# Kernel optimization log

Measured on AMD Instinct MI355X. Metric: run time of the kernel, lower is better.

Reference implementation:

```python
import jax, jax.numpy as jnp
import numpy as np

B, T, D = 2, 2048, 2048
H, HKV, RD = 16, 4, 64
DH = D // H          # 128
REP = H // HKV       # 4
NEG = -1e30


def _apply_rope(x, cos, sin, rd):
    # x: (B, h, T, Dh); cos/sin: (T, rd//2) broadcast over (B, h)
    xr, xp = x[..., :rd], x[..., rd:]
    x1, x2 = xr[..., ::2], xr[..., 1::2]
    rot = jnp.stack([x1 * cos - x2 * sin, x1 * sin + x2 * cos], axis=-1)
    rot = rot.reshape(x1.shape[:-1] + (rd,))
    return jnp.concatenate([rot, xp], axis=-1)


def setup_inputs() -> dict:
    key = jax.random.key(0)
    ks = jax.random.split(key, 6)
    x = jax.random.normal(ks[0], (B, T, D), dtype=jnp.float32)
    # rotary tables for the first RD dims (RD//2 frequency pairs)
    inv_freq = 1.0 / (10000.0 ** (np.arange(RD // 2, dtype=np.float32) / (RD // 2)))
    ang = np.arange(T, dtype=np.float32)[:, None] * inv_freq[None, :]  # (T, RD//2)
    cos = jnp.asarray(np.cos(ang), dtype=jnp.float32)
    sin = jnp.asarray(np.sin(ang), dtype=jnp.float32)
    s = 0.02
    Wq = jax.random.normal(ks[1], (H * DH, D), dtype=jnp.float32) * s
    Wk = jax.random.normal(ks[2], (HKV * DH, D), dtype=jnp.float32) * s
    Wv = jax.random.normal(ks[3], (HKV * DH, D), dtype=jnp.float32) * s
    Wo = jax.random.normal(ks[4], (D, D), dtype=jnp.float32) * s
    temp = jnp.full((H,), 1.0 / np.sqrt(DH), dtype=jnp.float32)
    return {"x": x, "cos": cos, "sin": sin, "Wq": Wq, "Wk": Wk, "Wv": Wv, "Wo": Wo, "temp": temp}


def reference(x, cos, sin, Wq, Wk, Wv, Wo, temp):
    Bt, Tt, _ = x.shape
    q = (x @ Wq.T).reshape(Bt, Tt, H, DH).transpose(0, 2, 1, 3)    # (B,H,T,Dh)
    k = (x @ Wk.T).reshape(Bt, Tt, HKV, DH).transpose(0, 2, 1, 3)  # (B,Hkv,T,Dh)
    v = (x @ Wv.T).reshape(Bt, Tt, HKV, DH).transpose(0, 2, 1, 3)
    k = jnp.repeat(k, REP, axis=1)  # GQA repeat_interleave -> (B,H,T,Dh)
    v = jnp.repeat(v, REP, axis=1)
    q = _apply_rope(q, cos, sin, RD)
    k = _apply_rope(k, cos, sin, RD)
    q = q * temp[None, :, None, None]
    # SDPA causal, with default 1/sqrt(Dh) scale on top of learned temp
    scores = jnp.einsum("bhqd,bhkd->bhqk", q, k) / np.sqrt(DH)
    causal = jnp.tril(jnp.ones((Tt, Tt), dtype=bool))
    scores = jnp.where(causal[None, None], scores, NEG)
    attn = jax.nn.softmax(scores, axis=-1)
    out = jnp.einsum("bhqk,bhkd->bhqd", attn, v)  # (B,H,T,Dh)
    out = out.transpose(0, 2, 1, 3).reshape(Bt, Tt, H * DH)
    return out @ Wo.T
```

## Files before the change

### kernel.cpp

```cpp
#include <hip/hip_runtime.h>
#include <hip/hip_bf16.h>
#include <math.h>

#define B_   2
#define T_   2048
#define D_   2048
#define H_   16
#define HKV_ 4
#define DH_  128
#define RD_  64
#define KD_  (HKV_ * DH_)
#define SQKV 3072
#define VOFF 2560

typedef __attribute__((ext_vector_type(8))) short  short8;
typedef __attribute__((ext_vector_type(4))) short  short4v;
typedef __attribute__((ext_vector_type(4))) float  floatx4;

__device__ __forceinline__ void async16(const __hip_bfloat16* g, __hip_bfloat16* l) {
  __builtin_amdgcn_global_load_lds(
      (const __attribute__((address_space(1))) void*)g,
      (__attribute__((address_space(3))) void*)l, 16, 0, 0);
}

__device__ __forceinline__ short bf16b(float x) {
  union { __hip_bfloat16 h; short s; } u;
  u.h = __float2bfloat16(x);
  return u.s;
}

struct ConvArgs {
  const float* src[5];
  __hip_bfloat16* dst[5];
  int n[5];
};

__global__ __launch_bounds__(256) void conv_bf16(ConvArgs a) {
  const int arr = blockIdx.y;
  const int i = (blockIdx.x * 256 + threadIdx.x) * 8;
  if (i >= a.n[arr]) return;
  const float4 f1 = *(const float4*)(a.src[arr] + i);
  const float4 f2 = *(const float4*)(a.src[arr] + i + 4);
  union { short8 v; __hip_bfloat16 h[8]; } o;
  o.h[0] = __float2bfloat16(f1.x); o.h[1] = __float2bfloat16(f1.y);
  o.h[2] = __float2bfloat16(f1.z); o.h[3] = __float2bfloat16(f1.w);
  o.h[4] = __float2bfloat16(f2.x); o.h[5] = __float2bfloat16(f2.y);
  o.h[6] = __float2bfloat16(f2.z); o.h[7] = __float2bfloat16(f2.w);
  *(short8*)(a.dst[arr] + i) = o.v;
}

template <int MODE>
__global__ __launch_bounds__(512, 2) void gemm_8ph(const __hip_bfloat16* __restrict__ A,
                                                   const __hip_bfloat16* __restrict__ Bw,
                                                   void* __restrict__ Cout,
                                                   __hip_bfloat16* __restrict__ vtout,
                                                   int M, int N, int K, int nwg_x) {
  __shared__ __hip_bfloat16 As[3][16 * 512];
  __shared__ __hip_bfloat16 Bs[3][16 * 512];

  const int tid  = threadIdx.x;
  const int lane = tid & 63;
  const int w    = tid >> 6;
  const int wm   = w >> 2, wn = w & 3;
  const int quad = lane >> 4, m16 = lane & 15;

  const int nwg = gridDim.x;
  const int q8  = nwg >> 3, r8 = nwg & 7;
  const int xcd = blockIdx.x & 7, o8 = blockIdx.x >> 3;
  const int swz = (xcd < r8 ? xcd * (q8 + 1) : r8 * (q8 + 1) + (xcd - r8) * q8) + o8;
  const int bx = swz % nwg_x, by = swz / nwg_x;
  const int bm = by * 256, bn = bx * 256;

  const int rl = m16;
  const int kc = quad;
  const __hip_bfloat16* gA0 = A  + (size_t)(bm + (w * 2 + 0) * 16 + rl) * K + kc * 8;
  const __hip_bfloat16* gA1 = A  + (size_t)(bm + (w * 2 + 1) * 16 + rl) * K + kc * 8;
  const __hip_bfloat16* gB0 = Bw + (size_t)(bn + (w * 2 + 0) * 16 + rl) * K + kc * 8;
  const __hip_bfloat16* gB1 = Bw + (size_t)(bn + (w * 2 + 1) * 16 + rl) * K + kc * 8;

  const int nt = K >> 5;

  async16(gA0,      &As[0][(w * 2 + 0) * 512]);
  async16(gA1,      &As[0][(w * 2 + 1) * 512]);
  async16(gB0,      &Bs[0][(w * 2 + 0) * 512]);
  async16(gB1,      &Bs[0][(w * 2 + 1) * 512]);
  async16(gA0 + 32, &As[1][(w * 2 + 0) * 512]);
  async16(gA1 + 32, &As[1][(w * 2 + 1) * 512]);
  async16(gB0 + 32, &Bs[1][(w * 2 + 0) * 512]);
  async16(gB1 + 32, &Bs[1][(w * 2 + 1) * 512]);

  floatx4 acc[8][4] = {};
  const int fragoff = (quad * 16 + m16) * 8;

  int cur = 0, stg = 2;
  for (int t = 0; t < nt; ++t) {
    if (t < nt - 1) asm volatile("s_waitcnt vmcnt(4)" ::: "memory");
    else            asm volatile("s_waitcnt vmcnt(0)" ::: "memory");
    __builtin_amdgcn_s_barrier();
    __builtin_amdgcn_sched_barrier(0);

    const __hip_bfloat16* abase = &As[cur][0];
    const __hip_bfloat16* bbase = &Bs[cur][0];
    const bool doStage = (t + 2 < nt);
    const size_t ko = (size_t)(t + 2) * 32;

    short8 a0[4], b[4];
#pragma unroll
    for (int i = 0; i < 4; ++i) {
      a0[i] = *(const short8*)(abase + (wm * 8 + i) * 512 + fragoff);
      b[i]  = *(const short8*)(bbase + (wn * 4 + i) * 512 + fragoff);
    }
    if (doStage) {
      async16(gA0 + ko, &As[stg][(w * 2 + 0) * 512]);
      async16(gA1 + ko, &As[stg][(w * 2 + 1) * 512]);
    }
    __builtin_amdgcn_s_barrier();
    __builtin_amdgcn_sched_barrier(0);
    __builtin_amdgcn_s_setprio(1);
#pragma unroll
    for (int i = 0; i < 4; ++i)
#pragma unroll
      for (int j = 0; j < 4; ++j)
        acc[i][j] = __builtin_amdgcn_mfma_f32_16x16x32_bf16(a0[i], b[j], acc[i][j], 0, 0, 0);
    __builtin_amdgcn_s_setprio(0);
    __builtin_amdgcn_s_barrier();
    __builtin_amdgcn_sched_barrier(0);

    short8 a1[4];
#pragma unroll
    for (int i = 0; i < 4; ++i)
      a1[i] = *(const short8*)(abase + (wm * 8 + 4 + i) * 512 + fragoff);
    if (doStage) {
      async16(gB0 + ko, &Bs[stg][(w * 2 + 0) * 512]);
      async16(gB1 + ko, &Bs[stg][(w * 2 + 1) * 512]);
    }
    __builtin_amdgcn_s_barrier();
    __builtin_amdgcn_sched_barrier(0);
    __builtin_amdgcn_s_setprio(1);
#pragma unroll
    for (int i = 0; i < 4; ++i)
#pragma unroll
      for (int j = 0; j < 4; ++j)
        acc[4 + i][j] = __builtin_amdgcn_mfma_f32_16x16x32_bf16(a1[i], b[j], acc[4 + i][j], 0, 0, 0);
    __builtin_amdgcn_s_setprio(0);

    cur = (cur == 2) ? 0 : cur + 1;
    stg = (stg == 2) ? 0 : stg + 1;
  }

  if (MODE == 2 && bn >= VOFF) {
#pragma unroll
    for (int mt = 0; mt < 8; ++mt)
#pragma unroll
      for (int j = 0; j < 4; ++j) {
        const int dh = bn + wn * 64 + j * 16 + m16 - VOFF;
        const int row0 = bm + wm * 128 + mt * 16 + quad * 4;
        const int bb = row0 >> 11, t0 = row0 & (T_ - 1);
        short4v pk;
#pragma unroll
        for (int reg = 0; reg < 4; ++reg) pk[reg] = bf16b(acc[mt][j][reg]);
        *(short4v*)&vtout[((size_t)(bb * HKV_ + (dh >> 7)) * DH_ + (dh & 127)) * T_ + t0] = pk;
      }
    return;
  }

#pragma unroll
  for (int mt = 0; mt < 8; ++mt)
#pragma unroll
    for (int j = 0; j < 4; ++j)
#pragma unroll
      for (int reg = 0; reg < 4; ++reg) {
        const int row = bm + wm * 128 + mt * 16 + quad * 4 + reg;
        const int col = bn + wn * 64 + j * 16 + m16;
        if (MODE == 0)
          ((float*)Cout)[(size_t)row * N + col] = acc[mt][j][reg];
        else
          ((__hip_bfloat16*)Cout)[(size_t)row * N + col] = __float2bfloat16(acc[mt][j][reg]);
      }
}

__global__ __launch_bounds__(512, 2) void gemm_k1(const __hip_bfloat16* __restrict__ A,
                                                  const __hip_bfloat16* __restrict__ Bw,
                                                  float* __restrict__ Cout,
                                                  int M, int N, int K, int nwg_x) {
  __shared__ __hip_bfloat16 As[3][8 * 512];
  __shared__ __hip_bfloat16 Bs[3][16 * 512];

  const int tid  = threadIdx.x;
  const int lane = tid & 63;
  const int w    = tid >> 6;
  const int wm   = w >> 2, wn = w & 3;
  const int quad = lane >> 4, m16 = lane & 15;

  const int nwg = gridDim.x;
  const int q8  = nwg >> 3, r8 = nwg & 7;
  const int xcd = blockIdx.x & 7, o8 = blockIdx.x >> 3;
  const int swz = (xcd < r8 ? xcd * (q8 + 1) : r8 * (q8 + 1) + (xcd - r8) * q8) + o8;
  const int bx = swz % nwg_x, by = swz / nwg_x;
  const int bm = by * 128, bn = bx * 256;

  const __hip_bfloat16* gA  = A  + (size_t)(bm + w * 16 + m16) * K + quad * 8;
  const __hip_bfloat16* gB0 = Bw + (size_t)(bn + (w * 2 + 0) * 16 + m16) * K + quad * 8;
  const __hip_bfloat16* gB1 = Bw + (size_t)(bn + (w * 2 + 1) * 16 + m16) * K + quad * 8;

  const int nt = K >> 5;

  async16(gA,       &As[0][w * 512]);
  async16(gB0,      &Bs[0][(w * 2 + 0) * 512]);
  async16(gB1,      &Bs[0][(w * 2 + 1) * 512]);
  async16(gA + 32,  &As[1][w * 512]);
  async16(gB0 + 32, &Bs[1][(w * 2 + 0) * 512]);
  async16(gB1 + 32, &Bs[1][(w * 2 + 1) * 512]);

  floatx4 acc[4][4] = {};
  const int fragoff = (quad * 16 + m16) * 8;

  int cur = 0, stg = 2;
  for (int t = 0; t < nt; ++t) {
    if (t < nt - 1) asm volatile("s_waitcnt vmcnt(3)" ::: "memory");
    else            asm volatile("s_waitcnt vmcnt(0)" ::: "memory");
    __builtin_amdgcn_s_barrier();
    __builtin_amdgcn_sched_barrier(0);

    const __hip_bfloat16* abase = &As[cur][0];
    const __hip_bfloat16* bbase = &Bs[cur][0];

    short8 a[4], b[4];
#pragma unroll
    for (int i = 0; i < 4; ++i) {
      a[i] = *(const short8*)(abase + (wm * 4 + i) * 512 + fragoff);
      b[i] = *(const short8*)(bbase + (wn * 4 + i) * 512 + fragoff);
    }
    if (t + 2 < nt) {
      const size_t ko = (size_t)(t + 2) * 32;
      async16(gA + ko,  &As[stg][w * 512]);
      async16(gB0 + ko, &Bs[stg][(w * 2 + 0) * 512]);
      async16(gB1 + ko, &Bs[stg][(w * 2 + 1) * 512]);
    }
    __builtin_amdgcn_s_setprio(1);
#pragma unroll
    for (int i = 0; i < 4; ++i)
#pragma unroll
      for (int j = 0; j < 4; ++j)
        acc[i][j] = __builtin_amdgcn_mfma_f32_16x16x32_bf16(a[i], b[j], acc[i][j], 0, 0, 0);
    __builtin_amdgcn_s_setprio(0);

    cur = (cur == 2) ? 0 : cur + 1;
    stg = (stg == 2) ? 0 : stg + 1;
  }

#pragma unroll
  for (int mi = 0; mi < 4; ++mi)
#pragma unroll
    for (int nj = 0; nj < 4; ++nj)
#pragma unroll
      for (int reg = 0; reg < 4; ++reg) {
        const int row = bm + wm * 64 + mi * 16 + quad * 4 + reg;
        const int col = bn + wn * 64 + nj * 16 + m16;
        Cout[(size_t)row * N + col] = acc[mi][nj][reg];
      }
}

__global__ __launch_bounds__(256) void rope_qk(__hip_bfloat16* __restrict__ qkv,
                                               const float* __restrict__ cosT,
                                               const float* __restrict__ sinT,
                                               const float* __restrict__ temp,
                                               float inv_sqrt_dh) {
  const int unit = blockIdx.x * 4 + (threadIdx.x >> 6);
  const int lane = threadIdx.x & 63;
  const int M = B_ * T_;
  int bt, off;
  float scale;
  if (unit < M * H_) {
    const int h = unit % H_;
    bt = unit / H_;
    off = h * DH_;
    scale = temp[h] * inv_sqrt_dh;
  } else {
    const int u2 = unit - M * H_;
    const int h = u2 % HKV_;
    bt = u2 / HKV_;
    off = D_ + h * DH_;
    scale = 1.0f;
  }
  const int t = bt & (T_ - 1);
  __hip_bfloat16* p = qkv + (size_t)bt * SQKV + off;
  if (lane < 32) {
    const float x1 = __bfloat162float(p[2 * lane]);
    const float x2 = __bfloat162float(p[2 * lane + 1]);
    const float c = cosT[t * (RD_ / 2) + lane];
    const float s = sinT[t * (RD_ / 2) + lane];
    p[2 * lane]     = __float2bfloat16((x1 * c - x2 * s) * scale);
    p[2 * lane + 1] = __float2bfloat16((x1 * s + x2 * c) * scale);
  } else {
    const int d0 = RD_ + (lane - 32) * 2;
    p[d0]     = __float2bfloat16(__bfloat162float(p[d0]) * scale);
    p[d0 + 1] = __float2bfloat16(__bfloat162float(p[d0 + 1]) * scale);
  }
}

__global__ __launch_bounds__(512, 2) void flash_attn_t2(
    const __hip_bfloat16* __restrict__ qkv,
    const __hip_bfloat16* __restrict__ vt,
    __hip_bfloat16* __restrict__ ao) {
  __shared__ __hip_bfloat16 KV[2][16384];

  const int tid = threadIdx.x, lane = tid & 63, w = tid >> 6;
  const int quad = lane >> 4, m16 = lane & 15;

  const int bid = blockIdx.x;
  const int g = bid & 7;
  const int b = g >> 2, kvh = g & 3;
  const int u = bid >> 3;
  const int qt = 63 - u;
  const int hw = w & 3;
  const int khalf = w >> 2;
  const int h = kvh * 4 + hw;
  const int qRow0 = qt * 32;
  const int ktEnd = (qt >> 1) + 1;

  const size_t bT = (size_t)b * T_;

  short8 qa[2][4];
#pragma unroll
  for (int qi = 0; qi < 2; qi++) {
    const __hip_bfloat16* qp = qkv + (bT + qRow0 + qi * 16 + m16) * SQKV + h * DH_;
#pragma unroll
    for (int ks = 0; ks < 4; ks++) qa[qi][ks] = *(const short8*)(qp + ks * 32 + quad * 8);
  }

  const short one = (short)0x3F80;
  const short4v ones4 = {one, one, one, one};

  const __hip_bfloat16* kptr[2];
  const __hip_bfloat16* vptr[2];
#pragma unroll
  for (int e = 0; e < 2; e++) {
    const int I = w * 2 + e;
    const int panelK = I >> 2, kcK = (I & 3) * 4 + quad;
    kptr[e] = qkv + D_ + (bT + panelK * 16 + m16) * SQKV + kvh * DH_ + kcK * 8;
    const int panelV = I >> 1, tc = (I & 1) * 4 + quad;
    vptr[e] = vt + ((size_t)(b * HKV_ + kvh) * DH_ + panelV * 16 + m16) * T_ + tc * 8;
  }

#pragma unroll
  for (int e = 0; e < 2; e++) {
    const int I = w * 2 + e;
    async16(kptr[e], &KV[0][I * 512]);
    async16(vptr[e], &KV[0][8192 + I * 512]);
    kptr[e] += (size_t)64 * SQKV;
    vptr[e] += 64;
  }

  floatx4 ot[8][2] = {};
  floatx4 lt[2] = {};

  for (int kt = 0; kt < ktEnd; kt++) {
    const int cur = kt & 1;
    __syncthreads();
    if (kt + 1 < ktEnd) {
      const int nxt = cur ^ 1;
#pragma unroll
      for (int e = 0; e < 2; e++) {
        const int I = w * 2 + e;
        async16(kptr[e], &KV[nxt][I * 512]);
        async16(vptr[e], &KV[nxt][8192 + I * 512]);
        kptr[e] += (size_t)64 * SQKV;
        vptr[e] += 64;
      }
    }

    const bool last = (kt == ktEnd - 1);
    if (last && khalf == 1 && ((qt & 1) == 0)) continue;

    floatx4 st[2][2] = {};
#pragma unroll
    for (int ki = 0; ki < 2; ki++) {
      const int kg = khalf * 2 + ki;
#pragma unroll
      for (int ks = 0; ks < 4; ks++) {
        const int unit = kg * 256 + (ks * 4 + quad) * 16 + m16;
        const short8 kf = *(const short8*)&KV[cur][unit * 8];
#pragma unroll
        for (int qi = 0; qi < 2; qi++)
          st[ki][qi] = __builtin_amdgcn_mfma_f32_16x16x32_bf16(kf, qa[qi][ks],
                                                               st[ki][qi], 0, 0, 0);
      }
    }

    if (last && khalf == (qt & 1)) {
#pragma unroll
      for (int ki = 0; ki < 2; ki++)
#pragma unroll
        for (int qi = 0; qi < 2; qi++) {
          const int rowg = qRow0 + qi * 16 + m16;
#pragma unroll
          for (int reg = 0; reg < 4; reg++) {
            const int keyg = kt * 64 + khalf * 32 + ki * 16 + quad * 4 + reg;
            if (keyg > rowg) st[ki][qi][reg] = -1e30f;
          }
        }
    }

    short4v pf[2][2];
#pragma unroll
    for (int ki = 0; ki < 2; ki++)
#pragma unroll
      for (int qi = 0; qi < 2; qi++) {
        short4v t;
#pragma unroll
        for (int reg = 0; reg < 4; reg++) t[reg] = bf16b(__expf(st[ki][qi][reg]));
        pf[ki][qi] = t;
      }

#pragma unroll
    for (int mi = 0; mi < 8; mi++)
#pragma unroll
      for (int ki = 0; ki < 2; ki++) {
        const int kg = khalf * 2 + ki;
        const int unit = mi * 128 + (kg * 2 + (quad >> 1)) * 16 + m16;
        const short4v vf = *(const short4v*)&KV[cur][8192 + unit * 8 + (quad & 1) * 4];
#pragma unroll
        for (int qi = 0; qi < 2; qi++)
          ot[mi][qi] = __builtin_amdgcn_mfma_f32_16x16x16bf16_1k(vf, pf[ki][qi],
                                                                 ot[mi][qi], 0, 0, 0);
      }
#pragma unroll
    for (int ki = 0; ki < 2; ki++)
#pragma unroll
      for (int qi = 0; qi < 2; qi++)
        lt[qi] = __builtin_amdgcn_mfma_f32_16x16x16bf16_1k(ones4, pf[ki][qi],
                                                           lt[qi], 0, 0, 0);
  }

  floatx4* scr = (floatx4*)&KV[0][0];
  __syncthreads();
  if (khalf == 1) {
#pragma unroll
    for (int mi = 0; mi < 6; mi++)
#pragma unroll
      for (int qi = 0; qi < 2; qi++)
        scr[((hw * 6 + mi) * 2 + qi) * 64 + lane] = ot[mi][qi];
  }
  __syncthreads();
  if (khalf == 0) {
#pragma unroll
    for (int mi = 0; mi < 6; mi++)
#pragma unroll
      for (int qi = 0; qi < 2; qi++)
        ot[mi][qi] += scr[((hw * 6 + mi) * 2 + qi) * 64 + lane];
  }
  __syncthreads();
  if (khalf == 1) {
#pragma unroll
    for (int j = 0; j < 2; j++)
#pragma unroll
      for (int qi = 0; qi < 2; qi++)
        scr[((hw * 2 + j) * 2 + qi) * 64 + lane] = ot[6 + j][qi];
#pragma unroll
    for (int qi = 0; qi < 2; qi++)
      scr[1024 + (hw * 2 + qi) * 64 + lane] = lt[qi];
  }
  __syncthreads();
  if (khalf == 0) {
#pragma unroll
    for (int j = 0; j < 2; j++)
#pragma unroll
      for (int qi = 0; qi < 2; qi++)
        ot[6 + j][qi] += scr[((hw * 2 + j) * 2 + qi) * 64 + lane];
#pragma unroll
    for (int qi = 0; qi < 2; qi++)
      lt[qi] += scr[1024 + (hw * 2 + qi) * 64 + lane];

#pragma unroll
    for (int qi = 0; qi < 2; qi++) {
      const float inv = 1.0f / lt[qi][0];
      const size_t gr = (bT + qRow0 + qi * 16 + m16) * D_ + h * DH_;
#pragma unroll
      for (int mi = 0; mi < 8; mi++) {
        short4v o;
#pragma unroll
        for (int reg = 0; reg < 4; reg++) o[reg] = bf16b(ot[mi][qi][reg] * inv);
        *(short4v*)&ao[gr + mi * 16 + quad * 4] = o;
      }
    }
  }
}

extern "C" void kernel_launch(void* const* d_in, const int* in_sizes, int n_in,
                              void* d_out, int out_size, void* d_ws, size_t ws_size,
                              hipStream_t stream) {
  const float* x    = (const float*)d_in[0];
  const float* cosT = (const float*)d_in[1];
  const float* sinT = (const float*)d_in[2];
  const float* Wq   = (const float*)d_in[3];
  const float* Wk   = (const float*)d_in[4];
  const float* Wv   = (const float*)d_in[5];
  const float* Wo   = (const float*)d_in[6];
  const float* temp = (const float*)d_in[7];
  float* out = (float*)d_out;

  const int M = B_ * T_;
  const size_t XN   = (size_t)M * D_;
  const size_t WQN  = (size_t)D_ * D_;
  const size_t WKN  = (size_t)KD_ * D_;
  const size_t QKVN = (size_t)M * SQKV;
  const size_t KN   = (size_t)M * KD_;

  __hip_bfloat16* ws = (__hip_bfloat16*)d_ws;
  __hip_bfloat16* xb    = ws;  ws += XN;
  __hip_bfloat16* wqkvb = ws;  ws += WQN + 2 * WKN;
  __hip_bfloat16* wob   = ws;  ws += WQN;
  __hip_bfloat16* qkvb  = ws;  ws += QKVN;
  __hip_bfloat16* vtb   = ws;  ws += KN;
  __hip_bfloat16* aob   = ws;  ws += XN;

  dim3 blk(256);

  ConvArgs ca;
  ca.src[0] = x;  ca.dst[0] = xb;                  ca.n[0] = (int)XN;
  ca.src[1] = Wq; ca.dst[1] = wqkvb;               ca.n[1] = (int)WQN;
  ca.src[2] = Wk; ca.dst[2] = wqkvb + WQN;         ca.n[2] = (int)WKN;
  ca.src[3] = Wv; ca.dst[3] = wqkvb + WQN + WKN;   ca.n[3] = (int)WKN;
  ca.src[4] = Wo; ca.dst[4] = wob;                 ca.n[4] = (int)WQN;
  conv_bf16<<<dim3(4096, 5), blk, 0, stream>>>(ca);

  gemm_8ph<2><<<dim3((SQKV / 256) * (M / 256)), dim3(512), 0, stream>>>(
      xb, wqkvb, qkvb, vtb, M, SQKV, D_, SQKV / 256);

  const float inv_sqrt_dh = 1.0f / sqrtf((float)DH_);
  rope_qk<<<(M * (H_ + HKV_)) / 4, blk, 0, stream>>>(qkvb, cosT, sinT, temp, inv_sqrt_dh);

  flash_attn_t2<<<512, dim3(512), 0, stream>>>(qkvb, vtb, aob);

  gemm_k1<<<dim3((D_ / 256) * (M / 128)), dim3(512), 0, stream>>>(
      aob, wob, out, M, D_, D_, D_ / 256);
}
```

Baseline: 323.4 us.

## Shrink QKV GEMM tiles to 128x128 with 4-wave blocks for better CU fill

Replaces the 256x256-tile, 512-thread QKV projection GEMM with a 128x128-tile, 256-thread variant. Each wave now computes a 64x64 sub-tile. The two-phase split of each K step and its extra barriers are removed, leaving one barrier per K step. The launch grows from 192 to 768 workgroups, so the 4096x3072 projection should occupy more of the CUs, at the cost of less operand reuse per tile and more total global/LDS traffic.

```diff
diff --git a/kernel.cpp b/kernel.cpp
--- a/kernel.cpp
+++ b/kernel.cpp
@@ -50,18 +50,18 @@
 }
 
 template <int MODE>
-__global__ __launch_bounds__(512, 2) void gemm_8ph(const __hip_bfloat16* __restrict__ A,
+__global__ __launch_bounds__(256, 3) void gemm_128(const __hip_bfloat16* __restrict__ A,
                                                    const __hip_bfloat16* __restrict__ Bw,
                                                    void* __restrict__ Cout,
                                                    __hip_bfloat16* __restrict__ vtout,
                                                    int M, int N, int K, int nwg_x) {
-  __shared__ __hip_bfloat16 As[3][16 * 512];
-  __shared__ __hip_bfloat16 Bs[3][16 * 512];
+  __shared__ __hip_bfloat16 As[3][8 * 512];
+  __shared__ __hip_bfloat16 Bs[3][8 * 512];
 
   const int tid  = threadIdx.x;
   const int lane = tid & 63;
   const int w    = tid >> 6;
-  const int wm   = w >> 2, wn = w & 3;
+  const int wm   = w >> 1, wn = w & 1;
   const int quad = lane >> 4, m16 = lane & 15;
 
   const int nwg = gridDim.x;
@@ -69,14 +69,12 @@
   const int xcd = blockIdx.x & 7, o8 = blockIdx.x >> 3;
   const int swz = (xcd < r8 ? xcd * (q8 + 1) : r8 * (q8 + 1) + (xcd - r8) * q8) + o8;
   const int bx = swz % nwg_x, by = swz / nwg_x;
-  const int bm = by * 256, bn = bx * 256;
-
-  const int rl = m16;
-  const int kc = quad;
-  const __hip_bfloat16* gA0 = A  + (size_t)(bm + (w * 2 + 0) * 16 + rl) * K + kc * 8;
-  const __hip_bfloat16* gA1 = A  + (size_t)(bm + (w * 2 + 1) * 16 + rl) * K + kc * 8;
-  const __hip_bfloat16* gB0 = Bw + (size_t)(bn + (w * 2 + 0) * 16 + rl) * K + kc * 8;
-  const __hip_bfloat16* gB1 = Bw + (size_t)(bn + (w * 2 + 1) * 16 + rl) * K + kc * 8;
+  const int bm = by * 128, bn = bx * 128;
+
+  const __hip_bfloat16* gA0 = A  + (size_t)(bm + (w * 2 + 0) * 16 + m16) * K + quad * 8;
+  const __hip_bfloat16* gA1 = A  + (size_t)(bm + (w * 2 + 1) * 16 + m16) * K + quad * 8;
+  const __hip_bfloat16* gB0 = Bw + (size_t)(bn + (w * 2 + 0) * 16 + m16) * K + quad * 8;
+  const __hip_bfloat16* gB1 = Bw + (size_t)(bn + (w * 2 + 1) * 16 + m16) * K + quad * 8;
 
   const int nt = K >> 5;
 
@@ -89,7 +87,7 @@
   async16(gB0 + 32, &Bs[1][(w * 2 + 0) * 512]);
   async16(gB1 + 32, &Bs[1][(w * 2 + 1) * 512]);
 
-  floatx4 acc[8][4] = {};
+  floatx4 acc[4][4] = {};
   const int fragoff = (quad * 16 + m16) * 8;
 
   int cur = 0, stg = 2;
@@ -101,47 +99,26 @@
 
     const __hip_bfloat16* abase = &As[cur][0];
     const __hip_bfloat16* bbase = &Bs[cur][0];
-    const bool doStage = (t + 2 < nt);
-    const size_t ko = (size_t)(t + 2) * 32;
-
-    short8 a0[4], b[4];
+
+    short8 a[4], b[4];
 #pragma unroll
     for (int i = 0; i < 4; ++i) {
-      a0[i] = *(const short8*)(abase + (wm * 8 + i) * 512 + fragoff);
-      b[i]  = *(const short8*)(bbase + (wn * 4 + i) * 512 + fragoff);
-    }
-    if (doStage) {
+      a[i] = *(const short8*)(abase + (wm * 4 + i) * 512 + fragoff);
+      b[i] = *(const short8*)(bbase + (wn * 4 + i) * 512 + fragoff);
+    }
+    if (t + 2 < nt) {
+      const size_t ko = (size_t)(t + 2) * 32;
       async16(gA0 + ko, &As[stg][(w * 2 + 0) * 512]);
       async16(gA1 + ko, &As[stg][(w * 2 + 1) * 512]);
-    }
-    __builtin_amdgcn_s_barrier();
-    __builtin_amdgcn_sched_barrier(0);
-    __builtin_amdgcn_s_setprio(1);
-#pragma unroll
-    for (int i = 0; i < 4; ++i)
-#pragma unroll
-      for (int j = 0; j < 4; ++j)
-        acc[i][j] = __builtin_amdgcn_mfma_f32_16x16x32_bf16(a0[i], b[j], acc[i][j], 0, 0, 0);
-    __builtin_amdgcn_s_setprio(0);
-    __builtin_amdgcn_s_barrier();
-    __builtin_amdgcn_sched_barrier(0);
-
-    short8 a1[4];
-#pragma unroll
-    for (int i = 0; i < 4; ++i)
-      a1[i] = *(const short8*)(abase + (wm * 8 + 4 + i) * 512 + fragoff);
-    if (doStage) {
       async16(gB0 + ko, &Bs[stg][(w * 2 + 0) * 512]);
       async16(gB1 + ko, &Bs[stg][(w * 2 + 1) * 512]);
     }
-    __builtin_amdgcn_s_barrier();
-    __builtin_amdgcn_sched_barrier(0);
     __builtin_amdgcn_s_setprio(1);
 #pragma unroll
     for (int i = 0; i < 4; ++i)
 #pragma unroll
       for (int j = 0; j < 4; ++j)
-        acc[4 + i][j] = __builtin_amdgcn_mfma_f32_16x16x32_bf16(a1[i], b[j], acc[4 + i][j], 0, 0, 0);
+        acc[i][j] = __builtin_amdgcn_mfma_f32_16x16x32_bf16(a[i], b[j], acc[i][j], 0, 0, 0);
     __builtin_amdgcn_s_setprio(0);
 
     cur = (cur == 2) ? 0 : cur + 1;
@@ -150,32 +127,32 @@
 
   if (MODE == 2 && bn >= VOFF) {
 #pragma unroll
-    for (int mt = 0; mt < 8; ++mt)
+    for (int mi = 0; mi < 4; ++mi)
 #pragma unroll
       for (int j = 0; j < 4; ++j) {
         const int dh = bn + wn * 64 + j * 16 + m16 - VOFF;
-        const int row0 = bm + wm * 128 + mt * 16 + quad * 4;
+        const int row0 = bm + wm * 64 + mi * 16 + quad * 4;
         const int bb = row0 >> 11, t0 = row0 & (T_ - 1);
         short4v pk;
 #pragma unroll
-        for (int reg = 0; reg < 4; ++reg) pk[reg] = bf16b(acc[mt][j][reg]);
+        for (int reg = 0; reg < 4; ++reg) pk[reg] = bf16b(acc[mi][j][reg]);
         *(short4v*)&vtout[((size_t)(bb * HKV_ + (dh >> 7)) * DH_ + (dh & 127)) * T_ + t0] = pk;
       }
     return;
   }
 
 #pragma unroll
-  for (int mt = 0; mt < 8; ++mt)
+  for (int mi = 0; mi < 4; ++mi)
 #pragma unroll
     for (int j = 0; j < 4; ++j)
 #pragma unroll
       for (int reg = 0; reg < 4; ++reg) {
-        const int row = bm + wm * 128 + mt * 16 + quad * 4 + reg;
+        const int row = bm + wm * 64 + mi * 16 + quad * 4 + reg;
         const int col = bn + wn * 64 + j * 16 + m16;
         if (MODE == 0)
-          ((float*)Cout)[(size_t)row * N + col] = acc[mt][j][reg];
+          ((float*)Cout)[(size_t)row * N + col] = acc[mi][j][reg];
         else
-          ((__hip_bfloat16*)Cout)[(size_t)row * N + col] = __float2bfloat16(acc[mt][j][reg]);
+          ((__hip_bfloat16*)Cout)[(size_t)row * N + col] = __float2bfloat16(acc[mi][j][reg]);
       }
 }
 
@@ -525,8 +502,8 @@
   ca.src[4] = Wo; ca.dst[4] = wob;                 ca.n[4] = (int)WQN;
   conv_bf16<<<dim3(4096, 5), blk, 0, stream>>>(ca);
 
-  gemm_8ph<2><<<dim3((SQKV / 256) * (M / 256)), dim3(512), 0, stream>>>(
-      xb, wqkvb, qkvb, vtb, M, SQKV, D_, SQKV / 256);
+  gemm_128<2><<<dim3((SQKV / 128) * (M / 128)), dim3(256), 0, stream>>>(
+      xb, wqkvb, qkvb, vtb, M, SQKV, D_, SQKV / 128);
 
   const float inv_sqrt_dh = 1.0f / sqrtf((float)DH_);
   rope_qk<<<(M * (H_ + HKV_)) / 4, blk, 0, stream>>>(qkvb, cosT, sinT, temp, inv_sqrt_dh);
```

Result: slower. 338.7 us (+4.7%).
